# Kernel tuning notes

Measured on AMD Instinct MI355X. Metric: run time of the kernel, lower is better.

## Reference

```python
import jax, jax.numpy as jnp
import numpy as np

B = 64        # graphs per batch
NP = 96       # nodes per graph
H = 64        # hid_size
IN_F = 32     # node feature dim
E_F = 16      # edge feature dim
DEG = 8       # avg degree
ENSEMBLE = 1


def _lin(key, fan_in, fan_out):
    return jax.random.normal(key, (fan_in, fan_out), jnp.float32) / np.float32(np.sqrt(fan_in))


def setup_inputs() -> dict:
    key = jax.random.key(0)
    ks = jax.random.split(key, 12)
    N = B * NP
    E = B * NP * DEG
    x = jax.random.normal(ks[0], (N, IN_F), jnp.float32)
    edge_attr = jax.random.normal(ks[1], (E, E_F), jnp.float32)
    # within-graph random edges (sorted per-graph blocks, like is_sorted=True)
    rng = np.random.default_rng(0)
    off = (np.arange(B) * NP)[:, None]
    src = (rng.integers(0, NP, size=(B, NP * DEG)) + off).ravel()
    dst = (rng.integers(0, NP, size=(B, NP * DEG)) + off).ravel()
    edge_index = jnp.asarray(np.stack([src, dst]), dtype=jnp.int32)
    # idx = concat of triu_indices(n, -n) per graph == ALL n^2 pairs per graph
    tri = np.triu_indices(NP, -NP)
    idx0 = jnp.asarray((tri[0][None, :] + off).ravel(), jnp.int32)  # [B*NP^2]
    idx1 = jnp.asarray((tri[1][None, :] + off).ravel(), jnp.int32)
    params = dict(
        W_atom=_lin(ks[2], IN_F, H), b_atom=jnp.zeros((H,), jnp.float32),
        W_bond=_lin(ks[3], E_F, H), b_bond=jnp.zeros((H,), jnp.float32),
        W_node=_lin(ks[4], H, H), b_node=jnp.zeros((H,), jnp.float32),
        W_edge=_lin(ks[5], H, H), b_edge=jnp.zeros((H,), jnp.float32),
        W1=_lin(ks[6], 3 * H, H), b1=jnp.zeros((H,), jnp.float32),
        W2=_lin(ks[7], H, H), b2=jnp.zeros((H,), jnp.float32),
        W3=_lin(ks[8], H, ENSEMBLE), b3=jnp.zeros((ENSEMBLE,), jnp.float32),
    )
    return dict(x=x, edge_attr=edge_attr, edge_index=edge_index,
                idx0=idx0, idx1=idx1, n=NP, **params)


def reference(x, edge_attr, edge_index, idx0, idx1, n,
              W_atom, b_atom, W_bond, b_bond, W_node, b_node,
              W_edge, b_edge, W1, b1, W2, b2, W3, b3):
    # encoders
    xh = x @ W_atom + b_atom                 # [N, H]
    eh = edge_attr @ W_bond + b_bond         # [E, H]
    emb_n = xh @ W_node + b_node             # [N, H]
    emb_e = eh @ W_edge + b_edge             # [E, H]
    # SparseTensor.to_dense() then gather at idx == scatter-add edge embeddings
    # into the per-graph dense pairwise slot (duplicates sum, missing = 0),
    # without materializing the O(N^2) adjacency.
    u, v = edge_index[0], edge_index[1]
    g = u // n
    pair_idx = g * (n * n) + (u - g * n) * n + (v - g * n)   # [E]
    P = idx0.shape[0]                         # B * n^2, idx enumerates all pairs row-major
    pair_e = jnp.zeros((P, emb_e.shape[1]), emb_e.dtype).at[pair_idx].add(emb_e)
    emb = jnp.concatenate((emb_n[idx0], emb_n[idx1], pair_e), axis=-1)  # [P, 3H]
    # MLP [3H, H, H, ensemble], plain last layer
    h = jax.nn.relu(emb @ W1 + b1)
    h = jax.nn.relu(h @ W2 + b2)
    return h @ W3 + b3                        # [P, ensemble]
```

## Files before the change

kernel.cpp:

```cpp
#include <hip/hip_runtime.h>
#if __has_include(<hip/hip_bf16.h>)
#include <hip/hip_bf16.h>
#define HAVE_BF16_H 1
#endif

#define NPG 96
#define BGR 64
#define HID 64
#define INF 32
#define EF  16
#define DEG 8
#define NN  (BGR*NPG)
#define NE  (BGR*NPG*DEG)
#define EPG (NPG*DEG)
#define PPG (NPG*NPG)
#define BMW 288

typedef short bf16x8 __attribute__((ext_vector_type(8)));
typedef float f32x4  __attribute__((ext_vector_type(4)));

__device__ __forceinline__ unsigned rne2(float lo, float hi) {
    union { float f; unsigned u; } a, b; a.f = lo; b.f = hi;
    unsigned ua = a.u + 0x7FFF + ((a.u >> 16) & 1);
    unsigned ub = b.u + 0x7FFF + ((b.u >> 16) & 1);
    return (ua >> 16) | (ub & 0xFFFF0000u);
}
__device__ __forceinline__ unsigned short rne1(float x) {
    union { float f; unsigned u; } a; a.f = x;
    return (unsigned short)((a.u + 0x7FFF + ((a.u >> 16) & 1)) >> 16);
}
__device__ __forceinline__ unsigned cvt2(float lo, float hi) {
#ifdef HAVE_BF16_H
    __hip_bfloat162 h2 = __float22bfloat162_rn(make_float2(lo, hi));
    unsigned u; __builtin_memcpy(&u, &h2, 4); return u;
#else
    return rne2(lo, hi);
#endif
}

__global__ __launch_bounds__(768) void prep_kernel(
    const float* __restrict__ x,
    const float* __restrict__ W_atom, const float* __restrict__ b_atom,
    const float* __restrict__ W_node, const float* __restrict__ b_node,
    const float* __restrict__ W1,     const float* __restrict__ b1,
    const float* __restrict__ ea,     const int* __restrict__ eidx,
    const float* __restrict__ W_bond, const float* __restrict__ b_bond,
    const float* __restrict__ W_edge, const float* __restrict__ b_edge,
    float* __restrict__ Abuf, float* __restrict__ Bbuf,
    int* __restrict__ fkey, int* __restrict__ fcnt,
    float* __restrict__ fsea, int* __restrict__ gcount,
    float* __restrict__ wec, float* __restrict__ biascg,
    unsigned* __restrict__ gbm)
{
    __shared__ __align__(16) char smem[45504];
    const int t = threadIdx.x;

    if (blockIdx.x >= 64) {
        float* sh = (float*)smem;
        const int wave = t >> 6, lane = t & 63;
        const int n = __builtin_amdgcn_readfirstlane((blockIdx.x - 64)*12 + wave);
        const float* xr = x + n * INF;

        float xh = b_atom[lane];
        #pragma unroll
        for (int k = 0; k < INF; ++k) xh += xr[k] * W_atom[k*HID + lane];
        sh[wave*64 + lane] = xh;
        __syncthreads();

        float en = b_node[lane];
        #pragma unroll
        for (int k = 0; k < HID; ++k) en += sh[wave*64 + k] * W_node[k*HID + lane];
        __syncthreads();
        sh[wave*64 + lane] = en;
        __syncthreads();

        float a = b1[lane], b = 0.f;
        #pragma unroll
        for (int k = 0; k < HID; ++k) {
            const float ek = sh[wave*64 + k];
            a += ek * W1[k*HID + lane];
            b += ek * W1[(HID + k)*HID + lane];
        }
        Abuf[n*HID + lane] = a;
        Bbuf[n*HID + lane] = b;
        return;
    }

    int*      head = (int*)smem;
    int*      nxt  = (int*)(smem + 36864);
    float*    sU   = (float*)(smem + 36864 + 3072);
    float*    sbe  = (float*)(smem + 36864 + 3072 + 4096);
    unsigned* bm   = (unsigned*)(smem + 36864+3072+4096+256);
    int*      lcnt = (int*)(smem + 36864+3072+4096+256+1152);
    const int g = blockIdx.x;

    for (int idx = t; idx < PPG; idx += EPG) head[idx] = -1;
    for (int idx = t; idx < BMW; idx += EPG) bm[idx] = 0u;
    if (t == 0) *lcnt = 0;

    const int u = eidx[g*EPG + t]      - g*NPG;
    const int v = eidx[NE + g*EPG + t] - g*NPG;
    const int key = u*NPG + v;
    __syncthreads();

    nxt[t] = atomicExch(&head[key], t);
    __syncthreads();

    if (head[key] == t) {
        const float* eag = ea + (size_t)g * EPG * EF;
        float s[EF];
        #pragma unroll
        for (int q = 0; q < EF; ++q) s[q] = 0.f;
        int cnt = 0;
        for (int e = t; e != -1; e = nxt[e]) {
            ++cnt;
            const float4* p = (const float4*)(eag + e*EF);
            #pragma unroll
            for (int q4 = 0; q4 < 4; ++q4) {
                const float4 f = p[q4];
                s[q4*4+0] += f.x; s[q4*4+1] += f.y;
                s[q4*4+2] += f.z; s[q4*4+3] += f.w;
            }
        }
        atomicOr(&bm[key >> 5], 1u << (key & 31));
        const int pos  = atomicAdd(lcnt, 1);
        const int slot = g*EPG + pos;
        fkey[slot] = key;
        fcnt[slot] = cnt;
        #pragma unroll
        for (int q = 0; q < EF; ++q) fsea[slot*EF + q] = s[q];
    }
    __syncthreads();
    for (int idx = t; idx < BMW; idx += EPG) gbm[g*BMW + idx] = bm[idx];
    if (t == 0) gcount[g] = *lcnt;

    if (g == 0) {
        for (int idx = t; idx < 16*64; idx += EPG) {
            const int r = idx >> 6, c = idx & 63;
            float s = 0.f;
            for (int k = 0; k < 64; ++k) s += W_bond[r*64+k] * W_edge[k*64+c];
            sU[idx] = s;
        }
        if (t < 64) {
            float s2 = b_edge[t];
            for (int k = 0; k < 64; ++k) s2 += b_bond[k] * W_edge[k*64+t];
            sbe[t] = s2;
        }
        __syncthreads();
        for (int idx = t; idx < 16*64; idx += EPG) {
            const int r = idx >> 6, c = idx & 63;
            float s = 0.f;
            for (int k = 0; k < 64; ++k) s += sU[r*64+k] * W1[(128+k)*64+c];
            wec[idx] = s;
        }
        if (t < 64) {
            float sc = 0.f;
            for (int k = 0; k < 64; ++k) sc += sbe[k] * W1[(128+k)*64+t];
            biascg[t] = sc;
        }
    }
}

#define SBST 68
#define W2ST 72
#define FIXW 16
__global__ __launch_bounds__(256) void pair_kernel(
    const float* __restrict__ Abuf, const float* __restrict__ Bbuf,
    const int* __restrict__ fkey, const int* __restrict__ fcnt,
    const float* __restrict__ fsea, const int* __restrict__ gcount,
    const float* __restrict__ wec,  const float* __restrict__ biascg,
    const unsigned* __restrict__ gbm,
    const float* __restrict__ W2,   const float* __restrict__ b2,
    const float* __restrict__ W3,   const float* __restrict__ b3,
    float* __restrict__ out)
{
    __shared__ __align__(16) char smem[37504];
    const int t = threadIdx.x;
    const int wave = t >> 6, lane = t & 63;
    const int col = lane & 15, q = lane >> 4;
    const float b3v = b3[0];

    if (blockIdx.x < 768) {
        float*          sB   = (float*)smem;
        float*          sA   = (float*)(smem + 26112);
        unsigned short* sW2t = (unsigned short*)(smem + 28160);
        unsigned*       sBM  = (unsigned*)(smem + 28160 + 9216);
        const int g  = blockIdx.x / 12;
        const int i0 = (blockIdx.x % 12) * 8;

        const float* Bg = Bbuf + g * NPG * 64;
        for (int idx = t; idx < NPG*64; idx += 256)
            sB[(idx >> 6)*SBST + (idx & 63)] = Bg[idx];
        for (int idx = t; idx < 8*64; idx += 256)
            sA[idx] = Abuf[(g*NPG + i0 + (idx >> 6))*64 + (idx & 63)];
        for (int idx = t; idx < 64*64; idx += 256) {
            const int k = idx >> 6, n = idx & 63;
            sW2t[n*W2ST + k] = rne1(W2[idx]);
        }
        if (t < 24) sBM[t] = gbm[g*BMW + i0*3 + t];
        __syncthreads();

        bf16x8 w2f[4][2];
        #pragma unroll
        for (int nt = 0; nt < 4; ++nt)
            #pragma unroll
            for (int c = 0; c < 2; ++c)
                w2f[nt][c] = *(const bf16x8*)(sW2t + (nt*16 + col)*W2ST + c*32 + q*8);

        float w3l[4], b2l[4];
        #pragma unroll
        for (int nt = 0; nt < 4; ++nt) {
            w3l[nt] = W3[nt*16 + col];
            b2l[nt] = b2[nt*16 + col];
        }

        #pragma unroll
        for (int ii = 0; ii < 2; ++ii) {
            const int il = wave*2 + ii;
            float areg[16];
            {
                const float4* Ar = (const float4*)(sA + il*64 + q*8);
                const float4 a0 = Ar[0], a1 = Ar[1];
                const float4 a2 = Ar[8], a3 = Ar[9];
                areg[0]=a0.x; areg[1]=a0.y; areg[2]=a0.z; areg[3]=a0.w;
                areg[4]=a1.x; areg[5]=a1.y; areg[6]=a1.z; areg[7]=a1.w;
                areg[8]=a2.x; areg[9]=a2.y; areg[10]=a2.z; areg[11]=a2.w;
                areg[12]=a3.x; areg[13]=a3.y; areg[14]=a3.z; areg[15]=a3.w;
            }
            float* outr = out + g*PPG + (i0 + il)*NPG;

            for (int jc = 0; jc < 6; ++jc) {
                const int j0 = jc * 16;
                union { bf16x8 v; unsigned u[4]; } h1[2];
                const float* Brow = sB + (j0 + col)*SBST + q*8;
                #pragma unroll
                for (int c = 0; c < 2; ++c) {
                    const float4 b0 = *(const float4*)(Brow + c*32);
                    const float4 b1v = *(const float4*)(Brow + c*32 + 4);
                    float h[8];
                    h[0] = fmaxf(areg[c*8+0] + b0.x, 0.f);
                    h[1] = fmaxf(areg[c*8+1] + b0.y, 0.f);
                    h[2] = fmaxf(areg[c*8+2] + b0.z, 0.f);
                    h[3] = fmaxf(areg[c*8+3] + b0.w, 0.f);
                    h[4] = fmaxf(areg[c*8+4] + b1v.x, 0.f);
                    h[5] = fmaxf(areg[c*8+5] + b1v.y, 0.f);
                    h[6] = fmaxf(areg[c*8+6] + b1v.z, 0.f);
                    h[7] = fmaxf(areg[c*8+7] + b1v.w, 0.f);
                    #pragma unroll
                    for (int p2 = 0; p2 < 4; ++p2)
                        h1[c].u[p2] = cvt2(h[2*p2], h[2*p2+1]);
                }
                f32x4 acc[4];
                #pragma unroll
                for (int nt = 0; nt < 4; ++nt) {
                    f32x4 z = {0.f, 0.f, 0.f, 0.f};
                    z = __builtin_amdgcn_mfma_f32_16x16x32_bf16(h1[0].v, w2f[nt][0], z, 0, 0, 0);
                    z = __builtin_amdgcn_mfma_f32_16x16x32_bf16(h1[1].v, w2f[nt][1], z, 0, 0, 0);
                    acc[nt] = z;
                }
                float p[4];
                #pragma unroll
                for (int r = 0; r < 4; ++r) {
                    float s = 0.f;
                    #pragma unroll
                    for (int nt = 0; nt < 4; ++nt)
                        s += fmaxf(acc[nt][r] + b2l[nt], 0.f) * w3l[nt];
                    p[r] = s;
                }
                #pragma unroll
                for (int off = 1; off < 16; off <<= 1) {
                    #pragma unroll
                    for (int r = 0; r < 4; ++r)
                        p[r] += __shfl_xor(p[r], off, 64);
                }
                if (col < 4) {
                    const int j = j0 + q*4 + col;
                    float pv = p[0];
                    pv = (col == 1) ? p[1] : pv;
                    pv = (col == 2) ? p[2] : pv;
                    pv = (col == 3) ? p[3] : pv;
                    if (!((sBM[il*3 + (j >> 5)] >> (j & 31)) & 1u))
                        outr[j] = pv + b3v;
                }
            }
        }
        return;
    }

    unsigned short* sW2t = (unsigned short*)smem;
    float*          sWEc = (float*)(smem + 9216);
    float*          sbc  = (float*)(smem + 9216 + 4096);

    for (int idx = t; idx < 64*64; idx += 256) {
        const int k = idx >> 6, n = idx & 63;
        sW2t[n*W2ST + k] = rne1(W2[idx]);
    }
    for (int idx = t; idx < 16*64; idx += 256) sWEc[idx] = wec[idx];
    if (t < 64) sbc[t] = biascg[t];
    __syncthreads();

    const int fb = blockIdx.x - 768;
    const int s0 = (fb * 4 + wave) * FIXW;
    const int g  = s0 / EPG;
    const int l0 = s0 % EPG;
    const int cg = gcount[g];
    if (l0 >= cg) return;

    bf16x8 w2f[4][2];
    #pragma unroll
    for (int nt = 0; nt < 4; ++nt)
        #pragma unroll
        for (int c = 0; c < 2; ++c)
            w2f[nt][c] = *(const bf16x8*)(sW2t + (nt*16 + col)*W2ST + c*32 + q*8);

    float w3l[4], b2l[4];
    #pragma unroll
    for (int nt = 0; nt < 4; ++nt) {
        w3l[nt] = W3[nt*16 + col];
        b2l[nt] = b2[nt*16 + col];
    }
    const int k0 = q * 8;

    union { bf16x8 v; unsigned u[4]; } h1[2];
    #pragma unroll
    for (int p2 = 0; p2 < 4; ++p2) { h1[0].u[p2] = 0; h1[1].u[p2] = 0; }

    const int s = s0 + col;
    if (l0 + col < cg) {
        const int key  = fkey[s];
        const float cf = (float)fcnt[s];
        const int ui = key / NPG, vi = key % NPG;

        float se[16];
        {
            const float4* p = (const float4*)(fsea + (size_t)s * EF);
            #pragma unroll
            for (int q4 = 0; q4 < 4; ++q4) {
                const float4 f = p[q4];
                se[q4*4+0] = f.x; se[q4*4+1] = f.y;
                se[q4*4+2] = f.z; se[q4*4+3] = f.w;
            }
        }

        float ck[16];
        #pragma unroll
        for (int kk = 0; kk < 8; ++kk) {
            ck[kk]     = cf * sbc[k0 + kk];
            ck[8 + kk] = cf * sbc[32 + k0 + kk];
        }
        #pragma unroll
        for (int qq = 0; qq < 16; ++qq) {
            const float sq = se[qq];
            const float4 w0 = *(const float4*)(sWEc + qq*64 + k0);
            const float4 w1 = *(const float4*)(sWEc + qq*64 + k0 + 4);
            const float4 w2v = *(const float4*)(sWEc + qq*64 + k0 + 32);
            const float4 w3v = *(const float4*)(sWEc + qq*64 + k0 + 36);
            ck[0]  += sq * w0.x;  ck[1]  += sq * w0.y;
            ck[2]  += sq * w0.z;  ck[3]  += sq * w0.w;
            ck[4]  += sq * w1.x;  ck[5]  += sq * w1.y;
            ck[6]  += sq * w1.z;  ck[7]  += sq * w1.w;
            ck[8]  += sq * w2v.x; ck[9]  += sq * w2v.y;
            ck[10] += sq * w2v.z; ck[11] += sq * w2v.w;
            ck[12] += sq * w3v.x; ck[13] += sq * w3v.y;
            ck[14] += sq * w3v.z; ck[15] += sq * w3v.w;
        }

        const float* Ar = Abuf + (g*NPG + ui)*64;
        const float* Br = Bbuf + (g*NPG + vi)*64;
        const float4 a0 = *(const float4*)(Ar + k0);
        const float4 a1 = *(const float4*)(Ar + k0 + 4);
        const float4 a2 = *(const float4*)(Ar + k0 + 32);
        const float4 a3 = *(const float4*)(Ar + k0 + 36);
        const float4 c0 = *(const float4*)(Br + k0);
        const float4 c1 = *(const float4*)(Br + k0 + 4);
        const float4 c2 = *(const float4*)(Br + k0 + 32);
        const float4 c3 = *(const float4*)(Br + k0 + 36);

        float h[16];
        h[0]  = fmaxf(a0.x + c0.x + ck[0],  0.f);
        h[1]  = fmaxf(a0.y + c0.y + ck[1],  0.f);
        h[2]  = fmaxf(a0.z + c0.z + ck[2],  0.f);
        h[3]  = fmaxf(a0.w + c0.w + ck[3],  0.f);
        h[4]  = fmaxf(a1.x + c1.x + ck[4],  0.f);
        h[5]  = fmaxf(a1.y + c1.y + ck[5],  0.f);
        h[6]  = fmaxf(a1.z + c1.z + ck[6],  0.f);
        h[7]  = fmaxf(a1.w + c1.w + ck[7],  0.f);
        h[8]  = fmaxf(a2.x + c2.x + ck[8],  0.f);
        h[9]  = fmaxf(a2.y + c2.y + ck[9],  0.f);
        h[10] = fmaxf(a2.z + c2.z + ck[10], 0.f);
        h[11] = fmaxf(a2.w + c2.w + ck[11], 0.f);
        h[12] = fmaxf(a3.x + c3.x + ck[12], 0.f);
        h[13] = fmaxf(a3.y + c3.y + ck[13], 0.f);
        h[14] = fmaxf(a3.z + c3.z + ck[14], 0.f);
        h[15] = fmaxf(a3.w + c3.w + ck[15], 0.f);
        #pragma unroll
        for (int p2 = 0; p2 < 4; ++p2) {
            h1[0].u[p2] = cvt2(h[2*p2],     h[2*p2 + 1]);
            h1[1].u[p2] = cvt2(h[8 + 2*p2], h[8 + 2*p2 + 1]);
        }
    }

    f32x4 acc[4];
    #pragma unroll
    for (int nt = 0; nt < 4; ++nt) {
        f32x4 z = {0.f, 0.f, 0.f, 0.f};
        z = __builtin_amdgcn_mfma_f32_16x16x32_bf16(h1[0].v, w2f[nt][0], z, 0, 0, 0);
        z = __builtin_amdgcn_mfma_f32_16x16x32_bf16(h1[1].v, w2f[nt][1], z, 0, 0, 0);
        acc[nt] = z;
    }

    float p[4];
    #pragma unroll
    for (int r = 0; r < 4; ++r) {
        float sum = 0.f;
        #pragma unroll
        for (int nt = 0; nt < 4; ++nt)
            sum += fmaxf(acc[nt][r] + b2l[nt], 0.f) * w3l[nt];
        p[r] = sum;
    }
    #pragma unroll
    for (int off = 1; off < 16; off <<= 1) {
        #pragma unroll
        for (int r = 0; r < 4; ++r)
            p[r] += __shfl_xor(p[r], off, 64);
    }
    if (col < 4) {
        const int lr = q*4 + col;
        if (l0 + lr < cg) {
            float pv = p[0];
            pv = (col == 1) ? p[1] : pv;
            pv = (col == 2) ? p[2] : pv;
            pv = (col == 3) ? p[3] : pv;
            out[g*PPG + fkey[s0 + lr]] = pv + b3v;
        }
    }
}

extern "C" void kernel_launch(void* const* d_in, const int* in_sizes, int n_in,
                              void* d_out, int out_size, void* d_ws, size_t ws_size,
                              hipStream_t stream)
{
    const float* x      = (const float*)d_in[0];
    const float* ea     = (const float*)d_in[1];
    const int*   eidx   = (const int*)  d_in[2];
    const float* W_atom = (const float*)d_in[6];
    const float* b_atom = (const float*)d_in[7];
    const float* W_bond = (const float*)d_in[8];
    const float* b_bond = (const float*)d_in[9];
    const float* W_node = (const float*)d_in[10];
    const float* b_node = (const float*)d_in[11];
    const float* W_edge = (const float*)d_in[12];
    const float* b_edge = (const float*)d_in[13];
    const float* W1     = (const float*)d_in[14];
    const float* b1     = (const float*)d_in[15];
    const float* W2     = (const float*)d_in[16];
    const float* b2     = (const float*)d_in[17];
    const float* W3     = (const float*)d_in[18];
    const float* b3     = (const float*)d_in[19];
    float* out = (float*)d_out;

    float* ws    = (float*)d_ws;
    float* Abuf  = ws;
    float* Bbuf  = Abuf  + NN*HID;
    float* fsea  = Bbuf  + NN*HID;
    int*   fkey  = (int*)(fsea + NE*EF);
    int*   fcnt  = fkey + NE;
    int*   gcount= fcnt + NE;
    float* wec   = (float*)(gcount + BGR);
    float* biascg= wec + 16*64;
    unsigned* gbm= (unsigned*)(biascg + 64);

    prep_kernel<<<64 + NN/12, 768, 0, stream>>>(
        x, W_atom, b_atom, W_node, b_node, W1, b1,
        ea, eidx, W_bond, b_bond, W_edge, b_edge,
        Abuf, Bbuf, fkey, fcnt, fsea, gcount, wec, biascg, gbm);
    pair_kernel<<<768 + NE/(FIXW*4), 256, 0, stream>>>(
        Abuf, Bbuf, fkey, fcnt, fsea, gcount, wec, biascg, gbm,
        W2, b2, W3, b3, out);
}
```

Measured before the change: 141.0 us.

## Fuse prep and pair kernels into one per-graph-quarter kernel

Merges the two-kernel pipeline into a single kernel of 256 blocks, each owning a graph and a 24-row slice. Every block recomputes its graph's node embeddings and A/B projections, the combined edge weight matrix, and its own edge dedup in shared memory. This removes a kernel launch and the global round-trips for A/B buffers, bitmaps and keys. In exchange, node-projection and weight-fold work is repeated per block, and only 256 blocks of 512 threads with about 61KB of shared memory each run, which limits occupancy and parallelism.

```diff
diff --git a/kernel.cpp b/kernel.cpp
--- a/kernel.cpp
+++ b/kernel.cpp
@@ -14,7 +14,9 @@
 #define NE  (BGR*NPG*DEG)
 #define EPG (NPG*DEG)
 #define PPG (NPG*NPG)
-#define BMW 288
+#define ROWS 24
+#define SBST 68
+#define W2ST 72
 
 typedef short bf16x8 __attribute__((ext_vector_type(8)));
 typedef float f32x4  __attribute__((ext_vector_type(4)));
@@ -38,7 +40,7 @@
 #endif
 }
 
-__global__ __launch_bounds__(768) void prep_kernel(
+__global__ __launch_bounds__(512) void fused_kernel(
     const float* __restrict__ x,
     const float* __restrict__ W_atom, const float* __restrict__ b_atom,
     const float* __restrict__ W_node, const float* __restrict__ b_node,
@@ -46,265 +48,162 @@
     const float* __restrict__ ea,     const int* __restrict__ eidx,
     const float* __restrict__ W_bond, const float* __restrict__ b_bond,
     const float* __restrict__ W_edge, const float* __restrict__ b_edge,
-    float* __restrict__ Abuf, float* __restrict__ Bbuf,
-    int* __restrict__ fkey, int* __restrict__ fcnt,
-    float* __restrict__ fsea, int* __restrict__ gcount,
-    float* __restrict__ wec, float* __restrict__ biascg,
-    unsigned* __restrict__ gbm)
-{
-    __shared__ __align__(16) char smem[45504];
-    const int t = threadIdx.x;
-
-    if (blockIdx.x >= 64) {
-        float* sh = (float*)smem;
-        const int wave = t >> 6, lane = t & 63;
-        const int n = __builtin_amdgcn_readfirstlane((blockIdx.x - 64)*12 + wave);
-        const float* xr = x + n * INF;
-
-        float xh = b_atom[lane];
-        #pragma unroll
-        for (int k = 0; k < INF; ++k) xh += xr[k] * W_atom[k*HID + lane];
-        sh[wave*64 + lane] = xh;
-        __syncthreads();
-
-        float en = b_node[lane];
-        #pragma unroll
-        for (int k = 0; k < HID; ++k) en += sh[wave*64 + k] * W_node[k*HID + lane];
-        __syncthreads();
-        sh[wave*64 + lane] = en;
-        __syncthreads();
-
-        float a = b1[lane], b = 0.f;
-        #pragma unroll
-        for (int k = 0; k < HID; ++k) {
-            const float ek = sh[wave*64 + k];
-            a += ek * W1[k*HID + lane];
-            b += ek * W1[(HID + k)*HID + lane];
-        }
-        Abuf[n*HID + lane] = a;
-        Bbuf[n*HID + lane] = b;
-        return;
-    }
-
-    int*      head = (int*)smem;
-    int*      nxt  = (int*)(smem + 36864);
-    float*    sU   = (float*)(smem + 36864 + 3072);
-    float*    sbe  = (float*)(smem + 36864 + 3072 + 4096);
-    unsigned* bm   = (unsigned*)(smem + 36864+3072+4096+256);
-    int*      lcnt = (int*)(smem + 36864+3072+4096+256+1152);
-    const int g = blockIdx.x;
-
-    for (int idx = t; idx < PPG; idx += EPG) head[idx] = -1;
-    for (int idx = t; idx < BMW; idx += EPG) bm[idx] = 0u;
-    if (t == 0) *lcnt = 0;
-
-    const int u = eidx[g*EPG + t]      - g*NPG;
-    const int v = eidx[NE + g*EPG + t] - g*NPG;
-    const int key = u*NPG + v;
-    __syncthreads();
-
-    nxt[t] = atomicExch(&head[key], t);
-    __syncthreads();
-
-    if (head[key] == t) {
-        const float* eag = ea + (size_t)g * EPG * EF;
-        float s[EF];
-        #pragma unroll
-        for (int q = 0; q < EF; ++q) s[q] = 0.f;
-        int cnt = 0;
-        for (int e = t; e != -1; e = nxt[e]) {
-            ++cnt;
-            const float4* p = (const float4*)(eag + e*EF);
-            #pragma unroll
-            for (int q4 = 0; q4 < 4; ++q4) {
-                const float4 f = p[q4];
-                s[q4*4+0] += f.x; s[q4*4+1] += f.y;
-                s[q4*4+2] += f.z; s[q4*4+3] += f.w;
-            }
-        }
-        atomicOr(&bm[key >> 5], 1u << (key & 31));
-        const int pos  = atomicAdd(lcnt, 1);
-        const int slot = g*EPG + pos;
-        fkey[slot] = key;
-        fcnt[slot] = cnt;
-        #pragma unroll
-        for (int q = 0; q < EF; ++q) fsea[slot*EF + q] = s[q];
-    }
-    __syncthreads();
-    for (int idx = t; idx < BMW; idx += EPG) gbm[g*BMW + idx] = bm[idx];
-    if (t == 0) gcount[g] = *lcnt;
-
-    if (g == 0) {
-        for (int idx = t; idx < 16*64; idx += EPG) {
-            const int r = idx >> 6, c = idx & 63;
-            float s = 0.f;
-            for (int k = 0; k < 64; ++k) s += W_bond[r*64+k] * W_edge[k*64+c];
-            sU[idx] = s;
-        }
-        if (t < 64) {
-            float s2 = b_edge[t];
-            for (int k = 0; k < 64; ++k) s2 += b_bond[k] * W_edge[k*64+t];
-            sbe[t] = s2;
-        }
-        __syncthreads();
-        for (int idx = t; idx < 16*64; idx += EPG) {
-            const int r = idx >> 6, c = idx & 63;
-            float s = 0.f;
-            for (int k = 0; k < 64; ++k) s += sU[r*64+k] * W1[(128+k)*64+c];
-            wec[idx] = s;
-        }
-        if (t < 64) {
-            float sc = 0.f;
-            for (int k = 0; k < 64; ++k) sc += sbe[k] * W1[(128+k)*64+t];
-            biascg[t] = sc;
-        }
-    }
-}
-
-#define SBST 68
-#define W2ST 72
-#define FIXW 16
-__global__ __launch_bounds__(256) void pair_kernel(
-    const float* __restrict__ Abuf, const float* __restrict__ Bbuf,
-    const int* __restrict__ fkey, const int* __restrict__ fcnt,
-    const float* __restrict__ fsea, const int* __restrict__ gcount,
-    const float* __restrict__ wec,  const float* __restrict__ biascg,
-    const unsigned* __restrict__ gbm,
-    const float* __restrict__ W2,   const float* __restrict__ b2,
-    const float* __restrict__ W3,   const float* __restrict__ b3,
+    const float* __restrict__ W2,     const float* __restrict__ b2,
+    const float* __restrict__ W3,     const float* __restrict__ b3,
+    float* __restrict__ fseaG,
     float* __restrict__ out)
 {
-    __shared__ __align__(16) char smem[37504];
+    __shared__ __align__(16) char smem[61504];
+    float*          sB    = (float*)smem;
+    float*          sA    = (float*)(smem + 26112);
+    unsigned short* sW2t  = (unsigned short*)(smem + 32256);
+    float*          sWEc  = (float*)(smem + 41472);
+    float*          sbc   = (float*)(smem + 45568);
+    float*          sENh  = (float*)(smem + 45824);
+    float*          sU    = (float*)(smem + 45824);
+    float*          sbe   = (float*)(smem + 49920);
+    int*            head2 = (int*)(smem + 45824);
+    int*            nxt   = (int*)(smem + 55040);
+    int*            fkeyL = (int*)(smem + 58112);
+    unsigned*       bm24  = (unsigned*)(smem + 61184);
+    int*            lcnt  = (int*)(smem + 61472);
+
     const int t = threadIdx.x;
     const int wave = t >> 6, lane = t & 63;
     const int col = lane & 15, q = lane >> 4;
+    const int g  = blockIdx.x >> 2;
+    const int r0 = (blockIdx.x & 3) * ROWS;
     const float b3v = b3[0];
 
-    if (blockIdx.x < 768) {
-        float*          sB   = (float*)smem;
-        float*          sA   = (float*)(smem + 26112);
-        unsigned short* sW2t = (unsigned short*)(smem + 28160);
-        unsigned*       sBM  = (unsigned*)(smem + 28160 + 9216);
-        const int g  = blockIdx.x / 12;
-        const int i0 = (blockIdx.x % 12) * 8;
-
-        const float* Bg = Bbuf + g * NPG * 64;
-        for (int idx = t; idx < NPG*64; idx += 256)
-            sB[(idx >> 6)*SBST + (idx & 63)] = Bg[idx];
-        for (int idx = t; idx < 8*64; idx += 256)
-            sA[idx] = Abuf[(g*NPG + i0 + (idx >> 6))*64 + (idx & 63)];
-        for (int idx = t; idx < 64*64; idx += 256) {
-            const int k = idx >> 6, n = idx & 63;
-            sW2t[n*W2ST + k] = rne1(W2[idx]);
-        }
-        if (t < 24) sBM[t] = gbm[g*BMW + i0*3 + t];
+    for (int half = 0; half < 2; ++half) {
+        const int nb = half * 48;
+        for (int rep = 0; rep < 6; ++rep) {
+            const int nl = wave*6 + rep;
+            const float* xr = x + (size_t)(g*NPG + nb + nl) * INF;
+            float xh = b_atom[lane];
+            #pragma unroll
+            for (int k = 0; k < INF; ++k) xh += xr[k] * W_atom[k*HID + lane];
+            sENh[nl*64 + lane] = xh;
+            float en = b_node[lane];
+            #pragma unroll
+            for (int k = 0; k < HID; ++k) en += sENh[nl*64 + k] * W_node[k*HID + lane];
+            sENh[nl*64 + lane] = en;
+        }
         __syncthreads();
-
-        bf16x8 w2f[4][2];
-        #pragma unroll
-        for (int nt = 0; nt < 4; ++nt)
-            #pragma unroll
-            for (int c = 0; c < 2; ++c)
-                w2f[nt][c] = *(const bf16x8*)(sW2t + (nt*16 + col)*W2ST + c*32 + q*8);
-
-        float w3l[4], b2l[4];
-        #pragma unroll
-        for (int nt = 0; nt < 4; ++nt) {
-            w3l[nt] = W3[nt*16 + col];
-            b2l[nt] = b2[nt*16 + col];
-        }
-
-        #pragma unroll
-        for (int ii = 0; ii < 2; ++ii) {
-            const int il = wave*2 + ii;
-            float areg[16];
-            {
-                const float4* Ar = (const float4*)(sA + il*64 + q*8);
-                const float4 a0 = Ar[0], a1 = Ar[1];
-                const float4 a2 = Ar[8], a3 = Ar[9];
-                areg[0]=a0.x; areg[1]=a0.y; areg[2]=a0.z; areg[3]=a0.w;
-                areg[4]=a1.x; areg[5]=a1.y; areg[6]=a1.z; areg[7]=a1.w;
-                areg[8]=a2.x; areg[9]=a2.y; areg[10]=a2.z; areg[11]=a2.w;
-                areg[12]=a3.x; areg[13]=a3.y; areg[14]=a3.z; areg[15]=a3.w;
-            }
-            float* outr = out + g*PPG + (i0 + il)*NPG;
-
-            for (int jc = 0; jc < 6; ++jc) {
-                const int j0 = jc * 16;
-                union { bf16x8 v; unsigned u[4]; } h1[2];
-                const float* Brow = sB + (j0 + col)*SBST + q*8;
+        for (int rep = 0; rep < 6; ++rep) {
+            const int rl = wave*6 + rep;
+            float bb = 0.f;
+            #pragma unroll
+            for (int k = 0; k < HID; ++k) bb += sENh[rl*64 + k] * W1[(HID + k)*HID + lane];
+            sB[(nb + rl)*SBST + lane] = bb;
+        }
+        if (r0 >= nb && r0 < nb + 48) {
+            #pragma unroll
+            for (int rep = 0; rep < 3; ++rep) {
+                const int i = wave*3 + rep;
+                const int rl = (r0 - nb) + i;
+                float a = b1[lane];
                 #pragma unroll
-                for (int c = 0; c < 2; ++c) {
-                    const float4 b0 = *(const float4*)(Brow + c*32);
-                    const float4 b1v = *(const float4*)(Brow + c*32 + 4);
-                    float h[8];
-                    h[0] = fmaxf(areg[c*8+0] + b0.x, 0.f);
-                    h[1] = fmaxf(areg[c*8+1] + b0.y, 0.f);
-                    h[2] = fmaxf(areg[c*8+2] + b0.z, 0.f);
-                    h[3] = fmaxf(areg[c*8+3] + b0.w, 0.f);
-                    h[4] = fmaxf(areg[c*8+4] + b1v.x, 0.f);
-                    h[5] = fmaxf(areg[c*8+5] + b1v.y, 0.f);
-                    h[6] = fmaxf(areg[c*8+6] + b1v.z, 0.f);
-                    h[7] = fmaxf(areg[c*8+7] + b1v.w, 0.f);
+                for (int k = 0; k < HID; ++k) a += sENh[rl*64 + k] * W1[k*HID + lane];
+                sA[i*64 + lane] = a;
+            }
+        }
+        __syncthreads();
+    }
+
+    for (int idx = t; idx < 4096; idx += 512)
+        sW2t[(idx & 63)*W2ST + (idx >> 6)] = rne1(W2[idx]);
+    { const int n = t >> 3, kk = 64 + (t & 7); sW2t[n*W2ST + kk] = 0; }
+
+    #pragma unroll
+    for (int ii2 = 0; ii2 < 2; ++ii2) {
+        const int idx = t + ii2*512;
+        const int r = idx >> 6, c = idx & 63;
+        float s = 0.f;
+        for (int k = 0; k < 64; ++k) s += W_bond[r*64 + k] * W_edge[k*64 + c];
+        sU[idx] = s;
+    }
+    if (t < 64) {
+        float s2 = b_edge[t];
+        for (int k = 0; k < 64; ++k) s2 += b_bond[k] * W_edge[k*64 + t];
+        sbe[t] = s2;
+    }
+    __syncthreads();
+    #pragma unroll
+    for (int ii2 = 0; ii2 < 2; ++ii2) {
+        const int idx = t + ii2*512;
+        const int r = idx >> 6, c = idx & 63;
+        float s = 0.f;
+        for (int k = 0; k < 64; ++k) s += sU[r*64 + k] * W1[(128 + k)*64 + c];
+        sWEc[idx] = s;
+    }
+    if (t < 64) {
+        float sc = 0.f;
+        for (int k = 0; k < 64; ++k) sc += sbe[k] * W1[(128 + k)*64 + t];
+        sbc[t] = sc;
+    }
+    __syncthreads();
+
+    for (int idx = t; idx < ROWS*NPG; idx += 512) head2[idx] = -1;
+    if (t < 72) bm24[t] = 0u;
+    if (t == 0) *lcnt = 0;
+
+    int eu[2], ev[2]; bool ein[2];
+    #pragma unroll
+    for (int c2 = 0; c2 < 2; ++c2) {
+        const int e = t + c2*512;
+        ein[c2] = false; eu[c2] = 0; ev[c2] = 0;
+        if (e < EPG) {
+            eu[c2] = eidx[g*EPG + e]      - g*NPG;
+            ev[c2] = eidx[NE + g*EPG + e] - g*NPG;
+            ein[c2] = (eu[c2] >= r0) && (eu[c2] < r0 + ROWS);
+        }
+    }
+    __syncthreads();
+
+    #pragma unroll
+    for (int c2 = 0; c2 < 2; ++c2) {
+        if (ein[c2]) {
+            const int e = t + c2*512;
+            const int key2 = (eu[c2] - r0)*NPG + ev[c2];
+            nxt[e] = atomicExch(&head2[key2], e);
+        }
+    }
+    __syncthreads();
+
+    {
+        const float* eag = ea + (size_t)g * EPG * EF;
+        #pragma unroll
+        for (int c2 = 0; c2 < 2; ++c2) {
+            if (ein[c2]) {
+                const int e0 = t + c2*512;
+                const int key2 = (eu[c2] - r0)*NPG + ev[c2];
+                if (head2[key2] == e0) {
+                    float s[EF];
                     #pragma unroll
-                    for (int p2 = 0; p2 < 4; ++p2)
-                        h1[c].u[p2] = cvt2(h[2*p2], h[2*p2+1]);
+                    for (int qq = 0; qq < EF; ++qq) s[qq] = 0.f;
+                    int cnt = 0;
+                    for (int e = e0; e != -1; e = nxt[e]) {
+                        ++cnt;
+                        const float4* p = (const float4*)(eag + e*EF);
+                        #pragma unroll
+                        for (int q4 = 0; q4 < 4; ++q4) {
+                            const float4 f = p[q4];
+                            s[q4*4+0] += f.x; s[q4*4+1] += f.y;
+                            s[q4*4+2] += f.z; s[q4*4+3] += f.w;
+                        }
+                    }
+                    atomicOr(&bm24[key2 >> 5], 1u << (key2 & 31));
+                    const int pos = atomicAdd(lcnt, 1);
+                    fkeyL[pos] = (eu[c2]*NPG + ev[c2]) | (cnt << 16);
+                    float* fp = fseaG + ((size_t)blockIdx.x * EPG + pos) * EF;
+                    #pragma unroll
+                    for (int qq = 0; qq < EF; ++qq) fp[qq] = s[qq];
                 }
-                f32x4 acc[4];
-                #pragma unroll
-                for (int nt = 0; nt < 4; ++nt) {
-                    f32x4 z = {0.f, 0.f, 0.f, 0.f};
-                    z = __builtin_amdgcn_mfma_f32_16x16x32_bf16(h1[0].v, w2f[nt][0], z, 0, 0, 0);
-                    z = __builtin_amdgcn_mfma_f32_16x16x32_bf16(h1[1].v, w2f[nt][1], z, 0, 0, 0);
-                    acc[nt] = z;
-                }
-                float p[4];
-                #pragma unroll
-                for (int r = 0; r < 4; ++r) {
-                    float s = 0.f;
-                    #pragma unroll
-                    for (int nt = 0; nt < 4; ++nt)
-                        s += fmaxf(acc[nt][r] + b2l[nt], 0.f) * w3l[nt];
-                    p[r] = s;
-                }
-                #pragma unroll
-                for (int off = 1; off < 16; off <<= 1) {
-                    #pragma unroll
-                    for (int r = 0; r < 4; ++r)
-                        p[r] += __shfl_xor(p[r], off, 64);
-                }
-                if (col < 4) {
-                    const int j = j0 + q*4 + col;
-                    float pv = p[0];
-                    pv = (col == 1) ? p[1] : pv;
-                    pv = (col == 2) ? p[2] : pv;
-                    pv = (col == 3) ? p[3] : pv;
-                    if (!((sBM[il*3 + (j >> 5)] >> (j & 31)) & 1u))
-                        outr[j] = pv + b3v;
-                }
-            }
-        }
-        return;
-    }
-
-    unsigned short* sW2t = (unsigned short*)smem;
-    float*          sWEc = (float*)(smem + 9216);
-    float*          sbc  = (float*)(smem + 9216 + 4096);
-
-    for (int idx = t; idx < 64*64; idx += 256) {
-        const int k = idx >> 6, n = idx & 63;
-        sW2t[n*W2ST + k] = rne1(W2[idx]);
-    }
-    for (int idx = t; idx < 16*64; idx += 256) sWEc[idx] = wec[idx];
-    if (t < 64) sbc[t] = biascg[t];
+            }
+        }
+    }
     __syncthreads();
-
-    const int fb = blockIdx.x - 768;
-    const int s0 = (fb * 4 + wave) * FIXW;
-    const int g  = s0 / EPG;
-    const int l0 = s0 % EPG;
-    const int cg = gcount[g];
-    if (l0 >= cg) return;
 
     bf16x8 w2f[4][2];
     #pragma unroll
@@ -319,119 +218,194 @@
         w3l[nt] = W3[nt*16 + col];
         b2l[nt] = b2[nt*16 + col];
     }
+
+    #pragma unroll
+    for (int rep = 0; rep < 3; ++rep) {
+        const int il = wave*3 + rep;
+        float areg[16];
+        {
+            const float4* Ar = (const float4*)(sA + il*64 + q*8);
+            const float4 a0 = Ar[0], a1 = Ar[1];
+            const float4 a2 = Ar[8], a3 = Ar[9];
+            areg[0]=a0.x; areg[1]=a0.y; areg[2]=a0.z; areg[3]=a0.w;
+            areg[4]=a1.x; areg[5]=a1.y; areg[6]=a1.z; areg[7]=a1.w;
+            areg[8]=a2.x; areg[9]=a2.y; areg[10]=a2.z; areg[11]=a2.w;
+            areg[12]=a3.x; areg[13]=a3.y; areg[14]=a3.z; areg[15]=a3.w;
+        }
+        float* outr = out + g*PPG + (r0 + il)*NPG;
+
+        for (int jc = 0; jc < 6; ++jc) {
+            const int j0 = jc * 16;
+            union { bf16x8 v; unsigned u[4]; } h1[2];
+            const float* Brow = sB + (j0 + col)*SBST + q*8;
+            #pragma unroll
+            for (int c = 0; c < 2; ++c) {
+                const float4 b0  = *(const float4*)(Brow + c*32);
+                const float4 b1v = *(const float4*)(Brow + c*32 + 4);
+                float h[8];
+                h[0] = fmaxf(areg[c*8+0] + b0.x, 0.f);
+                h[1] = fmaxf(areg[c*8+1] + b0.y, 0.f);
+                h[2] = fmaxf(areg[c*8+2] + b0.z, 0.f);
+                h[3] = fmaxf(areg[c*8+3] + b0.w, 0.f);
+                h[4] = fmaxf(areg[c*8+4] + b1v.x, 0.f);
+                h[5] = fmaxf(areg[c*8+5] + b1v.y, 0.f);
+                h[6] = fmaxf(areg[c*8+6] + b1v.z, 0.f);
+                h[7] = fmaxf(areg[c*8+7] + b1v.w, 0.f);
+                #pragma unroll
+                for (int p2 = 0; p2 < 4; ++p2)
+                    h1[c].u[p2] = cvt2(h[2*p2], h[2*p2+1]);
+            }
+            f32x4 acc[4];
+            #pragma unroll
+            for (int nt = 0; nt < 4; ++nt) {
+                f32x4 z = {0.f, 0.f, 0.f, 0.f};
+                z = __builtin_amdgcn_mfma_f32_16x16x32_bf16(h1[0].v, w2f[nt][0], z, 0, 0, 0);
+                z = __builtin_amdgcn_mfma_f32_16x16x32_bf16(h1[1].v, w2f[nt][1], z, 0, 0, 0);
+                acc[nt] = z;
+            }
+            float p[4];
+            #pragma unroll
+            for (int r = 0; r < 4; ++r) {
+                float s = 0.f;
+                #pragma unroll
+                for (int nt = 0; nt < 4; ++nt)
+                    s += fmaxf(acc[nt][r] + b2l[nt], 0.f) * w3l[nt];
+                p[r] = s;
+            }
+            #pragma unroll
+            for (int off = 1; off < 16; off <<= 1) {
+                #pragma unroll
+                for (int r = 0; r < 4; ++r)
+                    p[r] += __shfl_xor(p[r], off, 64);
+            }
+            if (col < 4) {
+                const int j = j0 + q*4 + col;
+                float pv = p[0];
+                pv = (col == 1) ? p[1] : pv;
+                pv = (col == 2) ? p[2] : pv;
+                pv = (col == 3) ? p[3] : pv;
+                if (!((bm24[il*3 + (j >> 5)] >> (j & 31)) & 1u))
+                    outr[j] = pv + b3v;
+            }
+        }
+    }
+
+    const int nk = *lcnt;
     const int k0 = q * 8;
-
-    union { bf16x8 v; unsigned u[4]; } h1[2];
-    #pragma unroll
-    for (int p2 = 0; p2 < 4; ++p2) { h1[0].u[p2] = 0; h1[1].u[p2] = 0; }
-
-    const int s = s0 + col;
-    if (l0 + col < cg) {
-        const int key  = fkey[s];
-        const float cf = (float)fcnt[s];
-        const int ui = key / NPG, vi = key % NPG;
-
-        float se[16];
-        {
-            const float4* p = (const float4*)(fsea + (size_t)s * EF);
-            #pragma unroll
-            for (int q4 = 0; q4 < 4; ++q4) {
-                const float4 f = p[q4];
-                se[q4*4+0] = f.x; se[q4*4+1] = f.y;
-                se[q4*4+2] = f.z; se[q4*4+3] = f.w;
-            }
-        }
-
-        float ck[16];
-        #pragma unroll
-        for (int kk = 0; kk < 8; ++kk) {
-            ck[kk]     = cf * sbc[k0 + kk];
-            ck[8 + kk] = cf * sbc[32 + k0 + kk];
-        }
-        #pragma unroll
-        for (int qq = 0; qq < 16; ++qq) {
-            const float sq = se[qq];
-            const float4 w0 = *(const float4*)(sWEc + qq*64 + k0);
-            const float4 w1 = *(const float4*)(sWEc + qq*64 + k0 + 4);
-            const float4 w2v = *(const float4*)(sWEc + qq*64 + k0 + 32);
-            const float4 w3v = *(const float4*)(sWEc + qq*64 + k0 + 36);
-            ck[0]  += sq * w0.x;  ck[1]  += sq * w0.y;
-            ck[2]  += sq * w0.z;  ck[3]  += sq * w0.w;
-            ck[4]  += sq * w1.x;  ck[5]  += sq * w1.y;
-            ck[6]  += sq * w1.z;  ck[7]  += sq * w1.w;
-            ck[8]  += sq * w2v.x; ck[9]  += sq * w2v.y;
-            ck[10] += sq * w2v.z; ck[11] += sq * w2v.w;
-            ck[12] += sq * w3v.x; ck[13] += sq * w3v.y;
-            ck[14] += sq * w3v.z; ck[15] += sq * w3v.w;
-        }
-
-        const float* Ar = Abuf + (g*NPG + ui)*64;
-        const float* Br = Bbuf + (g*NPG + vi)*64;
-        const float4 a0 = *(const float4*)(Ar + k0);
-        const float4 a1 = *(const float4*)(Ar + k0 + 4);
-        const float4 a2 = *(const float4*)(Ar + k0 + 32);
-        const float4 a3 = *(const float4*)(Ar + k0 + 36);
-        const float4 c0 = *(const float4*)(Br + k0);
-        const float4 c1 = *(const float4*)(Br + k0 + 4);
-        const float4 c2 = *(const float4*)(Br + k0 + 32);
-        const float4 c3 = *(const float4*)(Br + k0 + 36);
-
-        float h[16];
-        h[0]  = fmaxf(a0.x + c0.x + ck[0],  0.f);
-        h[1]  = fmaxf(a0.y + c0.y + ck[1],  0.f);
-        h[2]  = fmaxf(a0.z + c0.z + ck[2],  0.f);
-        h[3]  = fmaxf(a0.w + c0.w + ck[3],  0.f);
-        h[4]  = fmaxf(a1.x + c1.x + ck[4],  0.f);
-        h[5]  = fmaxf(a1.y + c1.y + ck[5],  0.f);
-        h[6]  = fmaxf(a1.z + c1.z + ck[6],  0.f);
-        h[7]  = fmaxf(a1.w + c1.w + ck[7],  0.f);
-        h[8]  = fmaxf(a2.x + c2.x + ck[8],  0.f);
-        h[9]  = fmaxf(a2.y + c2.y + ck[9],  0.f);
-        h[10] = fmaxf(a2.z + c2.z + ck[10], 0.f);
-        h[11] = fmaxf(a2.w + c2.w + ck[11], 0.f);
-        h[12] = fmaxf(a3.x + c3.x + ck[12], 0.f);
-        h[13] = fmaxf(a3.y + c3.y + ck[13], 0.f);
-        h[14] = fmaxf(a3.z + c3.z + ck[14], 0.f);
-        h[15] = fmaxf(a3.w + c3.w + ck[15], 0.f);
-        #pragma unroll
-        for (int p2 = 0; p2 < 4; ++p2) {
-            h1[0].u[p2] = cvt2(h[2*p2],     h[2*p2 + 1]);
-            h1[1].u[p2] = cvt2(h[8 + 2*p2], h[8 + 2*p2 + 1]);
-        }
-    }
-
-    f32x4 acc[4];
-    #pragma unroll
-    for (int nt = 0; nt < 4; ++nt) {
-        f32x4 z = {0.f, 0.f, 0.f, 0.f};
-        z = __builtin_amdgcn_mfma_f32_16x16x32_bf16(h1[0].v, w2f[nt][0], z, 0, 0, 0);
-        z = __builtin_amdgcn_mfma_f32_16x16x32_bf16(h1[1].v, w2f[nt][1], z, 0, 0, 0);
-        acc[nt] = z;
-    }
-
-    float p[4];
-    #pragma unroll
-    for (int r = 0; r < 4; ++r) {
-        float sum = 0.f;
-        #pragma unroll
-        for (int nt = 0; nt < 4; ++nt)
-            sum += fmaxf(acc[nt][r] + b2l[nt], 0.f) * w3l[nt];
-        p[r] = sum;
-    }
-    #pragma unroll
-    for (int off = 1; off < 16; off <<= 1) {
-        #pragma unroll
-        for (int r = 0; r < 4; ++r)
-            p[r] += __shfl_xor(p[r], off, 64);
-    }
-    if (col < 4) {
-        const int lr = q*4 + col;
-        if (l0 + lr < cg) {
-            float pv = p[0];
-            pv = (col == 1) ? p[1] : pv;
-            pv = (col == 2) ? p[2] : pv;
-            pv = (col == 3) ? p[3] : pv;
-            out[g*PPG + fkey[s0 + lr]] = pv + b3v;
+    for (int ch = wave; ch*16 < nk; ch += 8) {
+        union { bf16x8 v; unsigned u[4]; } h1[2];
+        #pragma unroll
+        for (int p2 = 0; p2 < 4; ++p2) { h1[0].u[p2] = 0; h1[1].u[p2] = 0; }
+
+        const int s = ch*16 + col;
+        if (s < nk) {
+            const int fk   = fkeyL[s];
+            const int key  = fk & 0xFFFF;
+            const float cf = (float)(fk >> 16);
+            const int ui = key / NPG, vi = key % NPG;
+
+            float se[16];
+            {
+                const float4* p = (const float4*)(fseaG + ((size_t)blockIdx.x * EPG + s) * EF);
+                #pragma unroll
+                for (int q4 = 0; q4 < 4; ++q4) {
+                    const float4 f = p[q4];
+                    se[q4*4+0] = f.x; se[q4*4+1] = f.y;
+                    se[q4*4+2] = f.z; se[q4*4+3] = f.w;
+                }
+            }
+
+            float ck[16];
+            #pragma unroll
+            for (int kk = 0; kk < 8; ++kk) {
+                ck[kk]     = cf * sbc[k0 + kk];
+                ck[8 + kk] = cf * sbc[32 + k0 + kk];
+            }
+            #pragma unroll
+            for (int qq = 0; qq < 16; ++qq) {
+                const float sq = se[qq];
+                const float4 w0  = *(const float4*)(sWEc + qq*64 + k0);
+                const float4 w1  = *(const float4*)(sWEc + qq*64 + k0 + 4);
+                const float4 w2v = *(const float4*)(sWEc + qq*64 + k0 + 32);
+                const float4 w3v = *(const float4*)(sWEc + qq*64 + k0 + 36);
+                ck[0]  += sq * w0.x;  ck[1]  += sq * w0.y;
+                ck[2]  += sq * w0.z;  ck[3]  += sq * w0.w;
+                ck[4]  += sq * w1.x;  ck[5]  += sq * w1.y;
+                ck[6]  += sq * w1.z;  ck[7]  += sq * w1.w;
+                ck[8]  += sq * w2v.x; ck[9]  += sq * w2v.y;
+                ck[10] += sq * w2v.z; ck[11] += sq * w2v.w;
+                ck[12] += sq * w3v.x; ck[13] += sq * w3v.y;
+                ck[14] += sq * w3v.z; ck[15] += sq * w3v.w;
+            }
+
+            const float* Ar = sA + (ui - r0)*64;
+            const float* Br = sB + vi*SBST;
+            const float4 a0 = *(const float4*)(Ar + k0);
+            const float4 a1 = *(const float4*)(Ar + k0 + 4);
+            const float4 a2 = *(const float4*)(Ar + k0 + 32);
+            const float4 a3 = *(const float4*)(Ar + k0 + 36);
+            const float4 c0 = *(const float4*)(Br + k0);
+            const float4 c1 = *(const float4*)(Br + k0 + 4);
+            const float4 c2 = *(const float4*)(Br + k0 + 32);
+            const float4 c3 = *(const float4*)(Br + k0 + 36);
+
+            float h[16];
+            h[0]  = fmaxf(a0.x + c0.x + ck[0],  0.f);
+            h[1]  = fmaxf(a0.y + c0.y + ck[1],  0.f);
+            h[2]  = fmaxf(a0.z + c0.z + ck[2],  0.f);
+            h[3]  = fmaxf(a0.w + c0.w + ck[3],  0.f);
+            h[4]  = fmaxf(a1.x + c1.x + ck[4],  0.f);
+            h[5]  = fmaxf(a1.y + c1.y + ck[5],  0.f);
+            h[6]  = fmaxf(a1.z + c1.z + ck[6],  0.f);
+            h[7]  = fmaxf(a1.w + c1.w + ck[7],  0.f);
+            h[8]  = fmaxf(a2.x + c2.x + ck[8],  0.f);
+            h[9]  = fmaxf(a2.y + c2.y + ck[9],  0.f);
+            h[10] = fmaxf(a2.z + c2.z + ck[10], 0.f);
+            h[11] = fmaxf(a2.w + c2.w + ck[11], 0.f);
+            h[12] = fmaxf(a3.x + c3.x + ck[12], 0.f);
+            h[13] = fmaxf(a3.y + c3.y + ck[13], 0.f);
+            h[14] = fmaxf(a3.z + c3.z + ck[14], 0.f);
+            h[15] = fmaxf(a3.w + c3.w + ck[15], 0.f);
+            #pragma unroll
+            for (int p2 = 0; p2 < 4; ++p2) {
+                h1[0].u[p2] = cvt2(h[2*p2],     h[2*p2 + 1]);
+                h1[1].u[p2] = cvt2(h[8 + 2*p2], h[8 + 2*p2 + 1]);
+            }
+        }
+
+        f32x4 acc[4];
+        #pragma unroll
+        for (int nt = 0; nt < 4; ++nt) {
+            f32x4 z = {0.f, 0.f, 0.f, 0.f};
+            z = __builtin_amdgcn_mfma_f32_16x16x32_bf16(h1[0].v, w2f[nt][0], z, 0, 0, 0);
+            z = __builtin_amdgcn_mfma_f32_16x16x32_bf16(h1[1].v, w2f[nt][1], z, 0, 0, 0);
+            acc[nt] = z;
+        }
+
+        float p[4];
+        #pragma unroll
+        for (int r = 0; r < 4; ++r) {
+            float sum = 0.f;
+            #pragma unroll
+            for (int nt = 0; nt < 4; ++nt)
+                sum += fmaxf(acc[nt][r] + b2l[nt], 0.f) * w3l[nt];
+            p[r] = sum;
+        }
+        #pragma unroll
+        for (int off = 1; off < 16; off <<= 1) {
+            #pragma unroll
+            for (int r = 0; r < 4; ++r)
+                p[r] += __shfl_xor(p[r], off, 64);
+        }
+        if (col < 4) {
+            const int lr = q*4 + col;
+            if (ch*16 + lr < nk) {
+                float pv = p[0];
+                pv = (col == 1) ? p[1] : pv;
+                pv = (col == 2) ? p[2] : pv;
+                pv = (col == 3) ? p[3] : pv;
+                out[g*PPG + (fkeyL[ch*16 + lr] & 0xFFFF)] = pv + b3v;
+            }
         }
     }
 }
@@ -459,22 +433,10 @@
     const float* b3     = (const float*)d_in[19];
     float* out = (float*)d_out;
 
-    float* ws    = (float*)d_ws;
-    float* Abuf  = ws;
-    float* Bbuf  = Abuf  + NN*HID;
-    float* fsea  = Bbuf  + NN*HID;
-    int*   fkey  = (int*)(fsea + NE*EF);
-    int*   fcnt  = fkey + NE;
-    int*   gcount= fcnt + NE;
-    float* wec   = (float*)(gcount + BGR);
-    float* biascg= wec + 16*64;
-    unsigned* gbm= (unsigned*)(biascg + 64);
-
-    prep_kernel<<<64 + NN/12, 768, 0, stream>>>(
+    float* fseaG = (float*)d_ws;
+
+    fused_kernel<<<BGR*4, 512, 0, stream>>>(
         x, W_atom, b_atom, W_node, b_node, W1, b1,
         ea, eidx, W_bond, b_bond, W_edge, b_edge,
-        Abuf, Bbuf, fkey, fcnt, fsea, gcount, wec, biascg, gbm);
-    pair_kernel<<<768 + NE/(FIXW*4), 256, 0, stream>>>(
-        Abuf, Bbuf, fkey, fcnt, fsea, gcount, wec, biascg, gbm,
-        W2, b2, W3, b3, out);
+        W2, b2, W3, b3, fseaG, out);
 }
```

After: 229.6 us. 62.9% more time.
